# Kernel tuning notes

Measured on AMD Instinct MI355X. Metric: run time of the kernel, lower is better.

## Reference

```python
import jax, jax.numpy as jnp
import numpy as np

N_NODES = 30000
NEG_SLOPE = 0.2  # PyG GATConv default leaky_relu slope


def gat_conv(x, src, dst, W, a_src, a_dst, b, num_nodes, concat):
    """One PyG-style GATConv layer (add_self_loops already applied to src/dst).
    x: [N, F_in]; W: [F_in, H*C]; a_src, a_dst: [H, C]; b: [H*C] or [C].
    """
    H, C = a_src.shape
    h = (x @ W).reshape(num_nodes, H, C)                     # [N, H, C]
    alpha_src = jnp.einsum('nhc,hc->nh', h, a_src)           # [N, H]
    alpha_dst = jnp.einsum('nhc,hc->nh', h, a_dst)           # [N, H]
    e = jax.nn.leaky_relu(alpha_src[src] + alpha_dst[dst], NEG_SLOPE)  # [E, H]
    # scatter-softmax over incoming edges of each dst node
    e_max = jax.ops.segment_max(e, dst, num_segments=num_nodes)        # [N, H]
    e_exp = jnp.exp(e - e_max[dst])                                    # [E, H]
    denom = jax.ops.segment_sum(e_exp, dst, num_segments=num_nodes)    # [N, H]
    alpha = e_exp / denom[dst]                                         # [E, H]
    msg = h[src] * alpha[:, :, None]                                   # [E, H, C]
    out = jax.ops.segment_sum(msg, dst, num_segments=num_nodes)        # [N, H, C]
    out = out.reshape(num_nodes, H * C) if concat else out.mean(axis=1)
    return out + b


def _glorot(key, shape):
    fan = sum(shape[:2]) if len(shape) > 1 else shape[0] * 2
    return jax.random.normal(key, shape, dtype=jnp.float32) * np.sqrt(2.0 / fan)


def setup_inputs() -> dict:
    key = jax.random.key(0)
    ks = jax.random.split(key, 16)
    n, f_in, heads = N_NODES, 256, 4
    x = jax.random.normal(ks[0], (n, f_in), dtype=jnp.float32)
    edge_index = jax.random.randint(ks[1], (2, 480000), 0, n, dtype=jnp.int64)
    inp = {
        'x': x, 'edge_index': edge_index,
        'W1': _glorot(ks[2], (f_in, heads * 128)),
        'a1s': _glorot(ks[3], (heads, 128)), 'a1d': _glorot(ks[4], (heads, 128)),
        'b1': jnp.zeros((heads * 128,), jnp.float32),
        'W2': _glorot(ks[5], (heads * 128, heads * 128)),
        'a2s': _glorot(ks[6], (heads, 128)), 'a2d': _glorot(ks[7], (heads, 128)),
        'b2': jnp.zeros((heads * 128,), jnp.float32),
        'W3': _glorot(ks[8], (heads * 128, heads * 64)),
        'a3s': _glorot(ks[9], (heads, 64)), 'a3d': _glorot(ks[10], (heads, 64)),
        'b3': jnp.zeros((heads * 64,), jnp.float32),
        # conv4: 256 -> 64, 1 head, mean (concat=False)
        'W4': _glorot(ks[11], (heads * 64, 64)),
        'a4s': _glorot(ks[12], (1, 64)), 'a4d': _glorot(ks[13], (1, 64)),
        'b4': jnp.zeros((64,), jnp.float32),
    }
    return inp


def reference(x, edge_index, W1, a1s, a1d, b1, W2, a2s, a2d, b2,
              W3, a3s, a3d, b3, W4, a4s, a4d, b4):
    n = x.shape[0]
    # PyG GATConv default add_self_loops=True
    loops = jnp.arange(n, dtype=edge_index.dtype)
    src = jnp.concatenate([edge_index[0], loops])
    dst = jnp.concatenate([edge_index[1], loops])
    h = jax.nn.relu(gat_conv(x, src, dst, W1, a1s, a1d, b1, n, True))
    h = jax.nn.relu(gat_conv(h, src, dst, W2, a2s, a2d, b2, n, True))
    h = jax.nn.relu(gat_conv(h, src, dst, W3, a3s, a3d, b3, n, True))
    h = jax.nn.relu(gat_conv(h, src, dst, W4, a4s, a4d, b4, n, False))
    return h
```

## Files before the change

### kernel.cpp

```cpp
#include <hip/hip_runtime.h>
#include <hip/hip_fp16.h>
#include <math.h>


typedef __attribute__((ext_vector_type(8))) __bf16 bf16x8;
typedef __attribute__((ext_vector_type(4))) float floatx4;
typedef __attribute__((ext_vector_type(8))) unsigned short usv8;
typedef __attribute__((ext_vector_type(4))) unsigned short usv4;

__device__ __forceinline__ unsigned short f2bf(float f) {
    unsigned int u = __float_as_uint(f);
    u += 0x7fff + ((u >> 16) & 1);
    return (unsigned short)(u >> 16);
}
__device__ __forceinline__ float bf2f(unsigned short u) {
    return __uint_as_float(((unsigned int)u) << 16);
}
__device__ __forceinline__ float lrelu(float e) {
    return (e > 0.f) ? e : 0.2f * e;
}
__device__ __forceinline__ void gload16(const void* g, void* l) {
    __builtin_amdgcn_global_load_lds(
        (const __attribute__((address_space(1))) void*)g,
        (__attribute__((address_space(3))) void*)l, 16, 0, 0);
}

static __global__ void zero_int(int* __restrict__ p, int n) {
    int i = blockIdx.x * blockDim.x + threadIdx.x;
    if (i < n) p[i] = 0;
}
static __global__ void zero_float(float* __restrict__ p, int n) {
    int i = blockIdx.x * blockDim.x + threadIdx.x;
    if (i < n) p[i] = 0.f;
}

static __global__ void hist_kernel(const int* __restrict__ ei, int e0, int n_nodes,
                                   int* __restrict__ counts) {
    int e = blockIdx.x * blockDim.x + threadIdx.x;
    int et = e0 + n_nodes;
    if (e >= et) return;
    int d = (e < e0) ? ei[e0 + e] : (e - e0);
    atomicAdd(&counts[d], 1);
}

static __global__ void scan_kernel(const int* __restrict__ counts,
                                   int* __restrict__ row_ptr,
                                   int* __restrict__ cursor, int n) {
    __shared__ int sdata[1024];
    int tid = threadIdx.x;
    int per = (n + 1023) / 1024;
    int start = tid * per;
    int stop = min(start + per, n);
    if (start > n) start = n;
    int s = 0;
    for (int i = start; i < stop; i++) s += counts[i];
    sdata[tid] = s;
    __syncthreads();
    for (int off = 1; off < 1024; off <<= 1) {
        int t = (tid >= off) ? sdata[tid - off] : 0;
        __syncthreads();
        sdata[tid] += t;
        __syncthreads();
    }
    int run = sdata[tid] - s;
    for (int i = start; i < stop; i++) {
        row_ptr[i] = run;
        cursor[i] = run;
        run += counts[i];
    }
    if (stop == n) row_ptr[n] = run;
}

static __global__ void scatter_kernel(const int* __restrict__ ei, int e0, int n_nodes,
                                      int* __restrict__ cursor,
                                      int* __restrict__ src_sorted) {
    int e = blockIdx.x * blockDim.x + threadIdx.x;
    int et = e0 + n_nodes;
    if (e >= et) return;
    int s, d;
    if (e < e0) { s = ei[e]; d = ei[e0 + e]; } else { s = e - e0; d = s; }
    int pos = atomicAdd(&cursor[d], 1);
    src_sorted[pos] = s;
}

static __global__ void convA_kernel(const float* __restrict__ X,
                                    unsigned short* __restrict__ A, int M, int K) {
    int idx = blockIdx.x * 256 + threadIdx.x;
    if (idx >= M * K) return;
    int m = idx / K, k = idx % K;
    float v = X[idx];
    unsigned short hi = f2bf(v);
    size_t base = (size_t)m * (2 * K);
    A[base + k] = hi;
    A[base + K + k] = f2bf(v - bf2f(hi));
}

__device__ __forceinline__ void convW_one(const float* W, unsigned short* BT,
                                          int idx, int K, int N) {
    int n = idx / K, k = idx % K;
    float v = (n < N) ? W[(size_t)k * N + n] : 0.f;
    unsigned short hi = f2bf(v);
    size_t base = (size_t)n * (2 * K);
    BT[base + k] = hi;
    BT[base + K + k] = f2bf(v - bf2f(hi));
}

static __global__ void convW_all(const float* __restrict__ W1, unsigned short* __restrict__ BT1,
                                 const float* __restrict__ W2, unsigned short* __restrict__ BT2,
                                 const float* __restrict__ W3, unsigned short* __restrict__ BT3,
                                 const float* __restrict__ W4, unsigned short* __restrict__ BT4) {
    int idx = blockIdx.x * 256 + threadIdx.x;
    if (idx < 131072) { convW_one(W1, BT1, idx, 256, 512); return; }
    idx -= 131072;
    if (idx < 262144) { convW_one(W2, BT2, idx, 512, 512); return; }
    idx -= 262144;
    if (idx < 131072) { convW_one(W3, BT3, idx, 512, 256); return; }
    idx -= 131072;
    if (idx < 32768)  { convW_one(W4, BT4, idx, 256, 64); }
}

#define BM 128
#define BN 128
#define BKK 64

__launch_bounds__(256, 2)
static __global__ void gemm_mfma(const unsigned short* __restrict__ A,
                                 const unsigned short* __restrict__ B,
                                 __half* __restrict__ C, int M, int K, int N,
                                 int xcols, int mblocks,
                                 const float* __restrict__ asv,
                                 const float* __restrict__ adv,
                                 float* __restrict__ as_out,
                                 float* __restrict__ ad_out,
                                 int Hh, int Cc) {
    __shared__ __align__(16) unsigned short lds[4 * BM * BKK];
    const int tid  = threadIdx.x;
    const int lane = tid & 63;
    const int wave = tid >> 6;

    const int id = blockIdx.x;
    const int band = id / (8 * xcols);
    const int rem = id - band * 8 * xcols;
    const int band_rows = min(8, mblocks - band * 8);
    const int ry = rem % band_rows;
    const int rx = rem / band_rows;
    const int r0 = (band * 8 + ry) * BM;
    const int c0 = rx * BN;

    const int wm = (wave >> 1) * 64;
    const int wn = (wave & 1) * 64;
    const int q   = lane >> 4;
    const int m16 = lane & 15;

    floatx4 acc[4][4];
#pragma unroll
    for (int i = 0; i < 4; i++)
#pragma unroll
        for (int j = 0; j < 4; j++) acc[i][j] = {0.f, 0.f, 0.f, 0.f};

    const size_t sA = (size_t)(2 * K);
    const size_t sB = (size_t)(2 * K);
    char* ldsb = (char*)lds;

#pragma unroll 1
    for (int k0 = 0; k0 < K; k0 += BKK) {
        __syncthreads();
#pragma unroll
        for (int c = 0; c < 4; c++) {
            int slot = c * 256 + tid;
            int row = slot >> 3;
            int gc  = (slot & 7) ^ (row & 7);
            const unsigned short* Ab = A + (size_t)(r0 + row) * sA + k0 + gc * 8;
            const unsigned short* Bb = B + (size_t)(c0 + row) * sB + k0 + gc * 8;
            gload16(Ab,     ldsb + slot * 16);
            gload16(Ab + K, ldsb + 16384 + slot * 16);
            gload16(Bb,     ldsb + 32768 + slot * 16);
            gload16(Bb + K, ldsb + 49152 + slot * 16);
        }
        __syncthreads();
#pragma unroll
        for (int ks = 0; ks < 2; ks++) {
            bf16x8 ah[4], al[4], bh[4], bl[4];
#pragma unroll
            for (int i = 0; i < 4; i++) {
                int row = wm + i * 16 + m16;
                int ch  = (q + ks * 4) ^ (row & 7);
                int off = (row * 8 + ch) * 16;
                ah[i] = *(const bf16x8*)(ldsb + off);
                al[i] = *(const bf16x8*)(ldsb + 16384 + off);
            }
#pragma unroll
            for (int j = 0; j < 4; j++) {
                int row = wn + j * 16 + m16;
                int ch  = (q + ks * 4) ^ (row & 7);
                int off = (row * 8 + ch) * 16;
                bh[j] = *(const bf16x8*)(ldsb + 32768 + off);
                bl[j] = *(const bf16x8*)(ldsb + 49152 + off);
            }
#pragma unroll
            for (int i = 0; i < 4; i++)
#pragma unroll
                for (int j = 0; j < 4; j++) {
                    acc[i][j] = __builtin_amdgcn_mfma_f32_16x16x32_bf16(
                        ah[i], bh[j], acc[i][j], 0, 0, 0);
                    acc[i][j] = __builtin_amdgcn_mfma_f32_16x16x32_bf16(
                        al[i], bh[j], acc[i][j], 0, 0, 0);
                    acc[i][j] = __builtin_amdgcn_mfma_f32_16x16x32_bf16(
                        ah[i], bl[j], acc[i][j], 0, 0, 0);
                }
        }
    }
#pragma unroll
    for (int i = 0; i < 4; i++)
#pragma unroll
        for (int j = 0; j < 4; j++)
#pragma unroll
            for (int r = 0; r < 4; r++) {
                int row = r0 + wm + i * 16 + q * 4 + r;
                int col = c0 + wn + j * 16 + m16;
                if (row < M && col < N)
                    C[(size_t)row * N + col] = __float2half(acc[i][j][r]);
            }
    if (c0 + wn < N) {
        int head = (c0 + wn) / Cc;
#pragma unroll
        for (int i = 0; i < 4; i++)
#pragma unroll
            for (int r = 0; r < 4; r++) {
                float ps = 0.f, pd = 0.f;
#pragma unroll
                for (int j = 0; j < 4; j++) {
                    int c = c0 + wn + j * 16 + m16;
                    float v = acc[i][j][r];
                    ps = fmaf(v, asv[c], ps);
                    pd = fmaf(v, adv[c], pd);
                }
#pragma unroll
                for (int off = 1; off < 16; off <<= 1) {
                    ps += __shfl_xor(ps, off);
                    pd += __shfl_xor(pd, off);
                }
                if (m16 == 0) {
                    int row = r0 + wm + i * 16 + q * 4 + r;
                    if (row < M) {
                        atomicAdd(&as_out[(size_t)row * Hh + head], ps);
                        atomicAdd(&ad_out[(size_t)row * Hh + head], pd);
                    }
                }
            }
    }
}

template <int R>
__device__ __forceinline__ void accum_row(const __half* hptr, size_t off, float w,
                                          float* acc) {
    const __half* p = hptr + off;
    if constexpr (R == 8) {
        float4 raw = *(const float4*)p;
        const __half2* hp = (const __half2*)&raw;
#pragma unroll
        for (int qq = 0; qq < 4; qq++) {
            float2 f = __half22float2(hp[qq]);
            acc[2 * qq + 0] += w * f.x;
            acc[2 * qq + 1] += w * f.y;
        }
    } else if constexpr (R == 4) {
        float2 raw = *(const float2*)p;
        const __half2* hp = (const __half2*)&raw;
#pragma unroll
        for (int qq = 0; qq < 2; qq++) {
            float2 f = __half22float2(hp[qq]);
            acc[2 * qq + 0] += w * f.x;
            acc[2 * qq + 1] += w * f.y;
        }
    } else {
        acc[0] += w * __half2float(*p);
    }
}

template <int H, int C, bool BF16OUT>
__launch_bounds__(256)
static __global__ void agg_kernel(const __half* __restrict__ h,
                                  const float* __restrict__ as_arr,
                                  const float* __restrict__ ad_arr,
                                  const int* __restrict__ row_ptr,
                                  const int* __restrict__ src_sorted,
                                  const float* __restrict__ bias,
                                  float* __restrict__ outf,
                                  unsigned short* __restrict__ outb, int n_nodes) {
    constexpr int R = H * C / 64;
    constexpr int G = 64 / H;
    constexpr int K = H * C;
    int wave = threadIdx.x >> 6;
    int lane = threadIdx.x & 63;
    int n = blockIdx.x * 4 + wave;
    if (n >= n_nodes) return;
    int beg = row_ptr[n], end = row_ptr[n + 1];

    float ad_h[H], m_h[H], l_h[H];
#pragma unroll
    for (int hh = 0; hh < H; hh++) {
        ad_h[hh] = ad_arr[(size_t)n * H + hh];
        m_h[hh] = -INFINITY;
        l_h[hh] = 0.f;
    }
    for (int base = beg; base < end; base += 64) {
        int j = base + lane;
        bool ok = j < end;
        float e_h[H];
        if (ok) {
            int s = src_sorted[j];
            if constexpr (H == 4) {
                float4 a = ((const float4*)as_arr)[s];
                e_h[0] = lrelu(a.x + ad_h[0]);
                e_h[1] = lrelu(a.y + ad_h[1]);
                e_h[2] = lrelu(a.z + ad_h[2]);
                e_h[3] = lrelu(a.w + ad_h[3]);
            } else {
                e_h[0] = lrelu(as_arr[s] + ad_h[0]);
            }
        } else {
#pragma unroll
            for (int hh = 0; hh < H; hh++) e_h[hh] = -INFINITY;
        }
#pragma unroll
        for (int hh = 0; hh < H; hh++) {
            float cm = e_h[hh];
#pragma unroll
            for (int off = 1; off < 64; off <<= 1) cm = fmaxf(cm, __shfl_xor(cm, off));
            float newm = fmaxf(m_h[hh], cm);
            float p = ok ? __expf(e_h[hh] - newm) : 0.f;
#pragma unroll
            for (int off = 1; off < 64; off <<= 1) p += __shfl_xor(p, off);
            l_h[hh] = l_h[hh] * __expf(m_h[hh] - newm) + p;
            m_h[hh] = newm;
        }
    }
    int myh = lane / G;
    float mm, adm, inv;
    if constexpr (H == 4) {
        mm  = m_h[0];  mm  = (myh == 1) ? m_h[1] : mm;  mm  = (myh == 2) ? m_h[2] : mm;  mm  = (myh == 3) ? m_h[3] : mm;
        float ll = l_h[0]; ll = (myh == 1) ? l_h[1] : ll; ll = (myh == 2) ? l_h[2] : ll; ll = (myh == 3) ? l_h[3] : ll;
        adm = ad_h[0]; adm = (myh == 1) ? ad_h[1] : adm; adm = (myh == 2) ? ad_h[2] : adm; adm = (myh == 3) ? ad_h[3] : adm;
        inv = 1.f / ll;
    } else {
        mm = m_h[0]; adm = ad_h[0]; inv = 1.f / l_h[0];
    }

    float acc[R];
#pragma unroll
    for (int r = 0; r < R; r++) acc[r] = 0.f;

    int j = beg;
    for (; j + 3 < end; j += 4) {
        int s0 = src_sorted[j];
        int s1 = src_sorted[j + 1];
        int s2 = src_sorted[j + 2];
        int s3 = src_sorted[j + 3];
        float w0 = __expf(lrelu(as_arr[(size_t)s0 * H + myh] + adm) - mm) * inv;
        float w1 = __expf(lrelu(as_arr[(size_t)s1 * H + myh] + adm) - mm) * inv;
        float w2 = __expf(lrelu(as_arr[(size_t)s2 * H + myh] + adm) - mm) * inv;
        float w3 = __expf(lrelu(as_arr[(size_t)s3 * H + myh] + adm) - mm) * inv;
        accum_row<R>(h, (size_t)s0 * K + lane * R, w0, acc);
        accum_row<R>(h, (size_t)s1 * K + lane * R, w1, acc);
        accum_row<R>(h, (size_t)s2 * K + lane * R, w2, acc);
        accum_row<R>(h, (size_t)s3 * K + lane * R, w3, acc);
    }
    for (; j < end; j++) {
        int s0 = src_sorted[j];
        float w0 = __expf(lrelu(as_arr[(size_t)s0 * H + myh] + adm) - mm) * inv;
        accum_row<R>(h, (size_t)s0 * K + lane * R, w0, acc);
    }

    float vout[R];
#pragma unroll
    for (int r = 0; r < R; r++)
        vout[r] = fmaxf(acc[r] + bias[lane * R + r], 0.f);

    if constexpr (BF16OUT) {
        unsigned short hi[R], lo[R];
#pragma unroll
        for (int r = 0; r < R; r++) {
            hi[r] = f2bf(vout[r]);
            lo[r] = f2bf(vout[r] - bf2f(hi[r]));
        }
        size_t base = (size_t)n * (2 * K) + lane * R;
        if constexpr (R == 8) {
            usv8 vh = {hi[0], hi[1], hi[2], hi[3], hi[4], hi[5], hi[6], hi[7]};
            usv8 vl = {lo[0], lo[1], lo[2], lo[3], lo[4], lo[5], lo[6], lo[7]};
            *(usv8*)(outb + base) = vh;
            *(usv8*)(outb + base + K) = vl;
        } else if constexpr (R == 4) {
            usv4 vh = {hi[0], hi[1], hi[2], hi[3]};
            usv4 vl = {lo[0], lo[1], lo[2], lo[3]};
            *(usv4*)(outb + base) = vh;
            *(usv4*)(outb + base + K) = vl;
        } else {
#pragma unroll
            for (int r = 0; r < R; r++) {
                outb[base + r] = hi[r];
                outb[base + K + r] = lo[r];
            }
        }
    } else {
#pragma unroll
        for (int r = 0; r < R; r++)
            outf[(size_t)n * K + lane * R + r] = vout[r];
    }
}


static inline size_t align_up(size_t x) { return (x + 255) & ~(size_t)255; }

extern "C" void kernel_launch(void* const* d_in, const int* in_sizes, int n_in,
                              void* d_out, int out_size, void* d_ws, size_t ws_size,
                              hipStream_t stream) {
    const float* x   = (const float*)d_in[0];
    const int*   ei  = (const int*)d_in[1];
    const float* W1  = (const float*)d_in[2];
    const float* a1s = (const float*)d_in[3];
    const float* a1d = (const float*)d_in[4];
    const float* b1  = (const float*)d_in[5];
    const float* W2  = (const float*)d_in[6];
    const float* a2s = (const float*)d_in[7];
    const float* a2d = (const float*)d_in[8];
    const float* b2  = (const float*)d_in[9];
    const float* W3  = (const float*)d_in[10];
    const float* a3s = (const float*)d_in[11];
    const float* a3d = (const float*)d_in[12];
    const float* b3  = (const float*)d_in[13];
    const float* W4  = (const float*)d_in[14];
    const float* a4s = (const float*)d_in[15];
    const float* a4d = (const float*)d_in[16];
    const float* b4  = (const float*)d_in[17];

    const int n  = in_sizes[0] / 256;
    const int e0 = in_sizes[1] / 2;
    const int et = e0 + n;
    const int Mpad = ((n + 127) / 128) * 128;

    char* w = (char*)d_ws;
    unsigned short* slotA = (unsigned short*)w;  w += align_up((size_t)Mpad * 1024 * 2);
    __half* hbuf = (__half*)w;                   w += align_up((size_t)n * 512 * 4);
    unsigned short* WT1 = (unsigned short*)w;    w += align_up((size_t)512 * 512 * 2);
    unsigned short* WT2 = (unsigned short*)w;    w += align_up((size_t)512 * 1024 * 2);
    unsigned short* WT3 = (unsigned short*)w;    w += align_up((size_t)256 * 1024 * 2);
    unsigned short* WT4 = (unsigned short*)w;    w += align_up((size_t)128 * 512 * 2);
    float* as_b = (float*)w;                     w += align_up((size_t)n * 4 * 4);
    float* ad_b = (float*)w;                     w += align_up((size_t)n * 4 * 4);
    int* row_ptr = (int*)w;                      w += align_up((size_t)(n + 1) * 4);
    int* counts  = (int*)w;                      w += align_up((size_t)n * 4);
    int* cursor  = (int*)w;                      w += align_up((size_t)n * 4);
    int* src_sorted = (int*)w;                   w += align_up((size_t)et * 4);
    (void)ws_size;

    dim3 blk(256);
    int nodeblocks = (n + 3) / 4;

    zero_int<<<(n + 255) / 256, 256, 0, stream>>>(counts, n);
    hist_kernel<<<(et + 255) / 256, 256, 0, stream>>>(ei, e0, n, counts);
    scan_kernel<<<1, 1024, 0, stream>>>(counts, row_ptr, cursor, n);
    scatter_kernel<<<(et + 255) / 256, 256, 0, stream>>>(ei, e0, n, cursor, src_sorted);

    convA_kernel<<<((n * 256) + 255) / 256, blk, 0, stream>>>(x, slotA, n, 256);
    convW_all<<<(557056 + 255) / 256, blk, 0, stream>>>(W1, WT1, W2, WT2, W3, WT3, W4, WT4);

    const int mblocks = Mpad / 128;
    const int zeroN = n * 8;

    zero_float<<<(zeroN + 255) / 256, blk, 0, stream>>>(as_b, zeroN);
    gemm_mfma<<<dim3(4 * mblocks), blk, 0, stream>>>(slotA, WT1, hbuf, n, 256, 512, 4, mblocks,
                                                     a1s, a1d, as_b, ad_b, 4, 128);
    agg_kernel<4, 128, true><<<nodeblocks, blk, 0, stream>>>(hbuf, as_b, ad_b, row_ptr, src_sorted, b1, nullptr, slotA, n);

    zero_float<<<(zeroN + 255) / 256, blk, 0, stream>>>(as_b, zeroN);
    gemm_mfma<<<dim3(4 * mblocks), blk, 0, stream>>>(slotA, WT2, hbuf, n, 512, 512, 4, mblocks,
                                                     a2s, a2d, as_b, ad_b, 4, 128);
    agg_kernel<4, 128, true><<<nodeblocks, blk, 0, stream>>>(hbuf, as_b, ad_b, row_ptr, src_sorted, b2, nullptr, slotA, n);

    zero_float<<<(zeroN + 255) / 256, blk, 0, stream>>>(as_b, zeroN);
    gemm_mfma<<<dim3(2 * mblocks), blk, 0, stream>>>(slotA, WT3, hbuf, n, 512, 256, 2, mblocks,
                                                     a3s, a3d, as_b, ad_b, 4, 64);
    agg_kernel<4, 64, true><<<nodeblocks, blk, 0, stream>>>(hbuf, as_b, ad_b, row_ptr, src_sorted, b3, nullptr, slotA, n);

    zero_float<<<(zeroN + 255) / 256, blk, 0, stream>>>(as_b, zeroN);
    gemm_mfma<<<dim3(1 * mblocks), blk, 0, stream>>>(slotA, WT4, hbuf, n, 256, 64, 1, mblocks,
                                                     a4s, a4d, as_b, ad_b, 1, 64);
    agg_kernel<1, 64, false><<<nodeblocks, blk, 0, stream>>>(hbuf, as_b, ad_b, row_ptr, src_sorted, b4, (float*)d_out, nullptr, n);
}
```

Baseline: 641.0 us.

## Cache edge logits in LDS and fuse next-layer zeroing into aggregation

The aggregation kernel now stores the leaky-relu edge logits computed in its softmax pass into a per-wave LDS buffer (up to 256 edges per node). The weighted-sum pass reads them back instead of re-gathering as_arr for each edge. The separate zero_float launches between layers are removed by ping-ponging two alpha buffers, with each agg kernel zeroing the next layer's buffer. The accumulate loop is also rewritten with explicit fmaf. The costs are extra LDS per block, which may lower occupancy, and a subtle ordering dependency on the ping-pong zeroing.

```diff
diff --git a/kernel.cpp b/kernel.cpp
--- a/kernel.cpp
+++ b/kernel.cpp
@@ -8,6 +8,8 @@
 typedef __attribute__((ext_vector_type(8))) unsigned short usv8;
 typedef __attribute__((ext_vector_type(4))) unsigned short usv4;
 
+#define DEG_CAP 256
+
 __device__ __forceinline__ unsigned short f2bf(float f) {
     unsigned int u = __float_as_uint(f);
     u += 0x7fff + ((u >> 16) & 1);
@@ -25,13 +27,13 @@
         (__attribute__((address_space(3))) void*)l, 16, 0, 0);
 }
 
+static __global__ void zero_float(float* __restrict__ p, int n) {
+    int i = blockIdx.x * blockDim.x + threadIdx.x;
+    if (i < n) p[i] = 0.f;
+}
 static __global__ void zero_int(int* __restrict__ p, int n) {
     int i = blockIdx.x * blockDim.x + threadIdx.x;
     if (i < n) p[i] = 0;
-}
-static __global__ void zero_float(float* __restrict__ p, int n) {
-    int i = blockIdx.x * blockDim.x + threadIdx.x;
-    if (i < n) p[i] = 0.f;
 }
 
 static __global__ void hist_kernel(const int* __restrict__ ei, int e0, int n_nodes,
@@ -257,24 +259,16 @@
     const __half* p = hptr + off;
     if constexpr (R == 8) {
         float4 raw = *(const float4*)p;
-        const __half2* hp = (const __half2*)&raw;
-#pragma unroll
-        for (int qq = 0; qq < 4; qq++) {
-            float2 f = __half22float2(hp[qq]);
-            acc[2 * qq + 0] += w * f.x;
-            acc[2 * qq + 1] += w * f.y;
-        }
+        const __half* hv = (const __half*)&raw;
+#pragma unroll
+        for (int r = 0; r < 8; r++) acc[r] = fmaf(__half2float(hv[r]), w, acc[r]);
     } else if constexpr (R == 4) {
         float2 raw = *(const float2*)p;
-        const __half2* hp = (const __half2*)&raw;
-#pragma unroll
-        for (int qq = 0; qq < 2; qq++) {
-            float2 f = __half22float2(hp[qq]);
-            acc[2 * qq + 0] += w * f.x;
-            acc[2 * qq + 1] += w * f.y;
-        }
+        const __half* hv = (const __half*)&raw;
+#pragma unroll
+        for (int r = 0; r < 4; r++) acc[r] = fmaf(__half2float(hv[r]), w, acc[r]);
     } else {
-        acc[0] += w * __half2float(*p);
+        acc[0] = fmaf(__half2float(*p), w, acc[0]);
     }
 }
 
@@ -287,15 +281,19 @@
                                   const int* __restrict__ src_sorted,
                                   const float* __restrict__ bias,
                                   float* __restrict__ outf,
-                                  unsigned short* __restrict__ outb, int n_nodes) {
+                                  unsigned short* __restrict__ outb,
+                                  float* __restrict__ znext_as,
+                                  float* __restrict__ znext_ad, int n_nodes) {
     constexpr int R = H * C / 64;
     constexpr int G = 64 / H;
     constexpr int K = H * C;
+    __shared__ float lds_e[4][DEG_CAP * H];
     int wave = threadIdx.x >> 6;
     int lane = threadIdx.x & 63;
     int n = blockIdx.x * 4 + wave;
     if (n >= n_nodes) return;
     int beg = row_ptr[n], end = row_ptr[n + 1];
+    float* we = lds_e[wave];
 
     float ad_h[H], m_h[H], l_h[H];
 #pragma unroll
@@ -319,6 +317,14 @@
             } else {
                 e_h[0] = lrelu(as_arr[s] + ad_h[0]);
             }
+            int idx = j - beg;
+            if (idx < DEG_CAP) {
+                if constexpr (H == 4) {
+                    *(float4*)&we[idx * 4] = make_float4(e_h[0], e_h[1], e_h[2], e_h[3]);
+                } else {
+                    we[idx] = e_h[0];
+                }
+            }
         } else {
 #pragma unroll
             for (int hh = 0; hh < H; hh++) e_h[hh] = -INFINITY;
@@ -353,25 +359,50 @@
 
     int j = beg;
     for (; j + 3 < end; j += 4) {
+        int i0 = j - beg;
         int s0 = src_sorted[j];
         int s1 = src_sorted[j + 1];
         int s2 = src_sorted[j + 2];
         int s3 = src_sorted[j + 3];
-        float w0 = __expf(lrelu(as_arr[(size_t)s0 * H + myh] + adm) - mm) * inv;
-        float w1 = __expf(lrelu(as_arr[(size_t)s1 * H + myh] + adm) - mm) * inv;
-        float w2 = __expf(lrelu(as_arr[(size_t)s2 * H + myh] + adm) - mm) * inv;
-        float w3 = __expf(lrelu(as_arr[(size_t)s3 * H + myh] + adm) - mm) * inv;
+        float e0, e1, e2, e3;
+        if (i0 + 3 < DEG_CAP) {
+            e0 = we[(i0 + 0) * H + myh];
+            e1 = we[(i0 + 1) * H + myh];
+            e2 = we[(i0 + 2) * H + myh];
+            e3 = we[(i0 + 3) * H + myh];
+        } else {
+            e0 = lrelu(as_arr[(size_t)s0 * H + myh] + adm);
+            e1 = lrelu(as_arr[(size_t)s1 * H + myh] + adm);
+            e2 = lrelu(as_arr[(size_t)s2 * H + myh] + adm);
+            e3 = lrelu(as_arr[(size_t)s3 * H + myh] + adm);
+        }
+        float w0 = __expf(e0 - mm) * inv;
+        float w1 = __expf(e1 - mm) * inv;
+        float w2 = __expf(e2 - mm) * inv;
+        float w3 = __expf(e3 - mm) * inv;
         accum_row<R>(h, (size_t)s0 * K + lane * R, w0, acc);
         accum_row<R>(h, (size_t)s1 * K + lane * R, w1, acc);
         accum_row<R>(h, (size_t)s2 * K + lane * R, w2, acc);
         accum_row<R>(h, (size_t)s3 * K + lane * R, w3, acc);
     }
     for (; j < end; j++) {
+        int i0 = j - beg;
         int s0 = src_sorted[j];
-        float w0 = __expf(lrelu(as_arr[(size_t)s0 * H + myh] + adm) - mm) * inv;
+        float e0 = (i0 < DEG_CAP) ? we[i0 * H + myh]
+                                  : lrelu(as_arr[(size_t)s0 * H + myh] + adm);
+        float w0 = __expf(e0 - mm) * inv;
         accum_row<R>(h, (size_t)s0 * K + lane * R, w0, acc);
     }
 
+    if (znext_as != nullptr && lane == 0) {
+        if constexpr (H == 4) {
+            *(float4*)&znext_as[(size_t)n * 4] = make_float4(0.f, 0.f, 0.f, 0.f);
+            *(float4*)&znext_ad[(size_t)n * 4] = make_float4(0.f, 0.f, 0.f, 0.f);
+        } else {
+            znext_as[n] = 0.f;
+            znext_ad[n] = 0.f;
+        }
+    }
     float vout[R];
 #pragma unroll
     for (int r = 0; r < R; r++)
@@ -446,8 +477,10 @@
     unsigned short* WT2 = (unsigned short*)w;    w += align_up((size_t)512 * 1024 * 2);
     unsigned short* WT3 = (unsigned short*)w;    w += align_up((size_t)256 * 1024 * 2);
     unsigned short* WT4 = (unsigned short*)w;    w += align_up((size_t)128 * 512 * 2);
-    float* as_b = (float*)w;                     w += align_up((size_t)n * 4 * 4);
-    float* ad_b = (float*)w;                     w += align_up((size_t)n * 4 * 4);
+    float* asA = (float*)w;                      w += align_up((size_t)n * 4 * 4);
+    float* adA = (float*)w;                      w += align_up((size_t)n * 4 * 4);
+    float* asB = (float*)w;                      w += align_up((size_t)n * 4 * 4);
+    float* adB = (float*)w;                      w += align_up((size_t)n * 4 * 4);
     int* row_ptr = (int*)w;                      w += align_up((size_t)(n + 1) * 4);
     int* counts  = (int*)w;                      w += align_up((size_t)n * 4);
     int* cursor  = (int*)w;                      w += align_up((size_t)n * 4);
@@ -464,27 +497,23 @@
 
     convA_kernel<<<((n * 256) + 255) / 256, blk, 0, stream>>>(x, slotA, n, 256);
     convW_all<<<(557056 + 255) / 256, blk, 0, stream>>>(W1, WT1, W2, WT2, W3, WT3, W4, WT4);
+    zero_float<<<(n * 8 + 255) / 256, blk, 0, stream>>>(asA, n * 8);
 
     const int mblocks = Mpad / 128;
-    const int zeroN = n * 8;
-
-    zero_float<<<(zeroN + 255) / 256, blk, 0, stream>>>(as_b, zeroN);
+
     gemm_mfma<<<dim3(4 * mblocks), blk, 0, stream>>>(slotA, WT1, hbuf, n, 256, 512, 4, mblocks,
-                                                     a1s, a1d, as_b, ad_b, 4, 128);
-    agg_kernel<4, 128, true><<<nodeblocks, blk, 0, stream>>>(hbuf, as_b, ad_b, row_ptr, src_sorted, b1, nullptr, slotA, n);
-
-    zero_float<<<(zeroN + 255) / 256, blk, 0, stream>>>(as_b, zeroN);
+                                                     a1s, a1d, asA, adA, 4, 128);
+    agg_kernel<4, 128, true><<<nodeblocks, blk, 0, stream>>>(hbuf, asA, adA, row_ptr, src_sorted, b1, nullptr, slotA, asB, adB, n);
+
     gemm_mfma<<<dim3(4 * mblocks), blk, 0, stream>>>(slotA, WT2, hbuf, n, 512, 512, 4, mblocks,
-                                                     a2s, a2d, as_b, ad_b, 4, 128);
-    agg_kernel<4, 128, true><<<nodeblocks, blk, 0, stream>>>(hbuf, as_b, ad_b, row_ptr, src_sorted, b2, nullptr, slotA, n);
-
-    zero_float<<<(zeroN + 255) / 256, blk, 0, stream>>>(as_b, zeroN);
+                                                     a2s, a2d, asB, adB, 4, 128);
+    agg_kernel<4, 128, true><<<nodeblocks, blk, 0, stream>>>(hbuf, asB, adB, row_ptr, src_sorted, b2, nullptr, slotA, asA, adA, n);
+
     gemm_mfma<<<dim3(2 * mblocks), blk, 0, stream>>>(slotA, WT3, hbuf, n, 512, 256, 2, mblocks,
-                                                     a3s, a3d, as_b, ad_b, 4, 64);
-    agg_kernel<4, 64, true><<<nodeblocks, blk, 0, stream>>>(hbuf, as_b, ad_b, row_ptr, src_sorted, b3, nullptr, slotA, n);
-
-    zero_float<<<(zeroN + 255) / 256, blk, 0, stream>>>(as_b, zeroN);
+                                                     a3s, a3d, asA, adA, 4, 64);
+    agg_kernel<4, 64, true><<<nodeblocks, blk, 0, stream>>>(hbuf, asA, adA, row_ptr, src_sorted, b3, nullptr, slotA, asB, adB, n);
+
     gemm_mfma<<<dim3(1 * mblocks), blk, 0, stream>>>(slotA, WT4, hbuf, n, 256, 64, 1, mblocks,
-                                                     a4s, a4d, as_b, ad_b, 1, 64);
-    agg_kernel<1, 64, false><<<nodeblocks, blk, 0, stream>>>(hbuf, as_b, ad_b, row_ptr, src_sorted, b4, (float*)d_out, nullptr, n);
-}
+                                                     a4s, a4d, asB, adB, 1, 64);
+    agg_kernel<1, 64, false><<<nodeblocks, blk, 0, stream>>>(hbuf, asB, adB, row_ptr, src_sorted, b4, (float*)d_out, nullptr, nullptr, nullptr, n);
+}
```

New measurement: 630.9 us. No clear change (-1.6%).
